# Kernel tuning notes

Measured on AMD Instinct MI355X. Metric: run time of the kernel, lower is better.

The kernel has to match this reference:

```python
import jax, jax.numpy as jnp
import numpy as np

N_NODES = 100000
N_EDGES = 1600000
IN_DIM = 128
HID = 128
BATCH = 16384


def gcn_conv(x, W, b, src, dst, norm, n_nodes):
    # PyG GCNConv: h = x @ W; aggregate norm-weighted messages; add bias.
    h = x @ W                      # [N, H]
    msg = h[src] * norm[:, None]   # [E+N, H] gather + scale
    out = jax.ops.segment_sum(msg, dst, num_segments=n_nodes)
    return out + b


def setup_inputs() -> dict:
    key = jax.random.key(0)
    ks = jax.random.split(key, 12)
    x = jax.random.normal(ks[0], (N_NODES, IN_DIM), dtype=jnp.float32)
    edge_index = jax.random.randint(ks[1], (2, N_EDGES), 0, N_NODES, dtype=jnp.int64)
    src_idx = jax.random.randint(ks[2], (BATCH,), 0, N_NODES, dtype=jnp.int64)
    tgt_idx = jax.random.randint(ks[3], (BATCH,), 0, N_NODES, dtype=jnp.int64)
    s = 1.0 / np.sqrt(HID)
    Wc0 = jax.random.uniform(ks[4], (IN_DIM, HID), jnp.float32, -s, s)
    Wc1 = jax.random.uniform(ks[5], (HID, HID), jnp.float32, -s, s)
    Wc2 = jax.random.uniform(ks[6], (HID, HID), jnp.float32, -s, s)
    bc0 = jnp.zeros((HID,), jnp.float32)
    bc1 = jnp.zeros((HID,), jnp.float32)
    bc2 = jnp.zeros((HID,), jnp.float32)
    s2 = 1.0 / np.sqrt(3 * HID)
    Ww = jax.random.uniform(ks[7], (3 * HID, HID), jnp.float32, -s2, s2)
    bw = jax.random.uniform(ks[8], (HID,), jnp.float32, -s2, s2)
    Wp = jax.random.uniform(ks[9], (3 * HID, HID), jnp.float32, -s2, s2)
    bp = jax.random.uniform(ks[10], (HID,), jnp.float32, -s2, s2)
    return {"x": x, "edge_index": edge_index, "src_idx": src_idx, "tgt_idx": tgt_idx,
            "Wc0": Wc0, "bc0": bc0, "Wc1": Wc1, "bc1": bc1, "Wc2": Wc2, "bc2": bc2,
            "Ww": Ww, "bw": bw, "Wp": Wp, "bp": bp}


def reference(x, edge_index, src_idx, tgt_idx, Wc0, bc0, Wc1, bc1, Wc2, bc2, Ww, bw, Wp, bp):
    n = x.shape[0]
    loops = jnp.arange(n, dtype=edge_index.dtype)
    src = jnp.concatenate([edge_index[0], loops])  # GCN adds self-loops
    dst = jnp.concatenate([edge_index[1], loops])
    deg = jax.ops.segment_sum(jnp.ones_like(src, dtype=x.dtype), dst, num_segments=n)
    dinv = jnp.where(deg > 0, jax.lax.rsqrt(deg), 0.0)
    norm = dinv[src] * dinv[dst]   # symmetric normalization D^-1/2 A D^-1/2

    x1 = jax.nn.relu(gcn_conv(x, Wc0, bc0, src, dst, norm, n))   # dropout p=0 -> identity
    x2 = jax.nn.relu(gcn_conv(x1, Wc1, bc1, src, dst, norm, n))
    x3 = jax.nn.relu(gcn_conv(x2, Wc2, bc2, src, dst, norm, n))
    xcat = jnp.concatenate([x1, x2, x3], axis=1)   # [N, 3H]
    xW = xcat @ Ww + bw   # [N, H]
    xp = xcat @ Wp + bp   # [N, H]
    # bilinear score: bmm of [B,1,H] x [B,H,1] == rowwise dot product
    sv = jnp.sum(xp[src_idx] * xW[tgt_idx], axis=-1)   # [B]
    return sv
```

## Files before the change

### kernel.cpp

```cpp
#include <hip/hip_runtime.h>
#include <hip/hip_bf16.h>

#define N_NODES 100000
#define N_EDGES 1600000
#define BATCH   16384
#define HID     128

#define SHIFT 9
#define BSZ   512
#define NB    196
#define EPB   8192

typedef __attribute__((ext_vector_type(8))) short bf16x8;
typedef __attribute__((ext_vector_type(4))) float fx4;
typedef __attribute__((ext_vector_type(2))) float fx2;

__device__ inline short f2bf(float f) {
    unsigned u = __builtin_bit_cast(unsigned, f);
    unsigned r = (u + 0x7FFF + ((u >> 16) & 1)) >> 16;
    return (short)r;
}
__device__ inline float bf2f(short s) {
    unsigned u = ((unsigned)(unsigned short)s) << 16;
    return __builtin_bit_cast(float, u);
}


__global__ __launch_bounds__(256) void k_bhist(const int* __restrict__ dst,
                                               int* __restrict__ bcnt, int E) {
    __shared__ int lh[NB];
    int t = threadIdx.x;
    for (int j = t; j < NB; j += 256) lh[j] = 0;
    __syncthreads();
    int base = blockIdx.x * 4096;
    int n = min(4096, E - base);
    for (int i = t; i < n; i += 256) atomicAdd(&lh[dst[base + i] >> SHIFT], 1);
    __syncthreads();
    for (int j = t; j < NB; j += 256)
        if (lh[j]) atomicAdd(&bcnt[j], lh[j]);
}

__global__ void k_bscan(const int* __restrict__ bcnt, int* __restrict__ bbase,
                        int* __restrict__ bcur, int* __restrict__ offsets) {
    __shared__ int sh[256];
    int t = threadIdx.x;
    int c = (t < NB) ? bcnt[t] : 0;
    sh[t] = c;
    __syncthreads();
    for (int off = 1; off < 256; off <<= 1) {
        int v = 0;
        if (t >= off) v = sh[t - off];
        __syncthreads();
        if (t >= off) sh[t] += v;
        __syncthreads();
    }
    int incl = sh[t];
    int excl = incl - c;
    if (t < NB) { bbase[t] = excl; bcur[t] = excl; }
    if (t == NB - 1) { bbase[NB] = incl; offsets[N_NODES] = incl; }
}

__global__ __launch_bounds__(256) void k_passA(
    const int* __restrict__ edge, int* __restrict__ bcur,
    unsigned* __restrict__ tmp, int E) {
    __shared__ unsigned staged[EPB];
    __shared__ unsigned char bkt[EPB];
    __shared__ int lh[NB], lstart[NB], gbase[NB], lcur[NB];
    int t = threadIdx.x;
    int base = blockIdx.x * EPB;
    int n = min(EPB, E - base);
    for (int j = t; j < NB; j += 256) lh[j] = 0;
    __syncthreads();
    for (int i = t; i < n; i += 256)
        atomicAdd(&lh[edge[E + base + i] >> SHIFT], 1);
    __syncthreads();
    if (t == 0) {
        int run = 0;
        for (int b = 0; b < NB; ++b) { lstart[b] = run; run += lh[b]; }
    }
    __syncthreads();
    if (t < NB) {
        gbase[t] = atomicAdd(&bcur[t], lh[t]);
        lcur[t] = lstart[t];
    }
    __syncthreads();
    for (int i = t; i < n; i += 256) {
        int s = edge[base + i];
        int d = edge[E + base + i];
        int b = d >> SHIFT;
        unsigned p = (unsigned)s | ((unsigned)(d & (BSZ - 1)) << 17);
        int pos = atomicAdd(&lcur[b], 1);
        staged[pos] = p;
        bkt[pos] = (unsigned char)b;
    }
    __syncthreads();
    for (int i = t; i < n; i += 256) {
        int b = bkt[i];
        tmp[gbase[b] + (i - lstart[b])] = staged[i];
    }
}

__global__ __launch_bounds__(256) void k_passB(
    const unsigned* __restrict__ tmp, const int* __restrict__ bbase,
    int* __restrict__ offsets, float* __restrict__ dinv,
    int* __restrict__ col) {
    __shared__ int lh[BSZ];
    __shared__ int lsum[256];
    int b = blockIdx.x, t = threadIdx.x;
    int begin = bbase[b], end = bbase[b + 1];
    lh[t] = 0; lh[t + 256] = 0;
    __syncthreads();
    for (int i = begin + t; i < end; i += 256)
        atomicAdd(&lh[tmp[i] >> 17], 1);
    __syncthreads();
    int c0 = lh[2 * t], c1 = lh[2 * t + 1];
    int tsum = c0 + c1;
    lsum[t] = tsum;
    __syncthreads();
    for (int off = 1; off < 256; off <<= 1) {
        int v = 0;
        if (t >= off) v = lsum[t - off];
        __syncthreads();
        if (t >= off) lsum[t] += v;
        __syncthreads();
    }
    int texcl = lsum[t] - tsum;
    int node0 = (b << SHIFT) + 2 * t;
    if (node0 < N_NODES) {
        offsets[node0] = begin + texcl;
        dinv[node0] = rsqrtf((float)c0 + 1.f);
    }
    if (node0 + 1 < N_NODES) {
        offsets[node0 + 1] = begin + texcl + c0;
        dinv[node0 + 1] = rsqrtf((float)c1 + 1.f);
    }
    __syncthreads();
    lh[2 * t] = texcl;
    lh[2 * t + 1] = texcl + c0;
    __syncthreads();
    for (int i = begin + t; i < end; i += 1024) {
        int i1 = i + 256, i2 = i + 512, i3 = i + 768;
        unsigned p0 = tmp[i];
        unsigned p1 = (i1 < end) ? tmp[i1] : 0u;
        unsigned p2 = (i2 < end) ? tmp[i2] : 0u;
        unsigned p3 = (i3 < end) ? tmp[i3] : 0u;
        int pos0 = begin + atomicAdd(&lh[p0 >> 17], 1);
        col[pos0] = (int)(p0 & 0x1FFFFu);
        if (i1 < end) { int q = begin + atomicAdd(&lh[p1 >> 17], 1); col[q] = (int)(p1 & 0x1FFFFu); }
        if (i2 < end) { int q = begin + atomicAdd(&lh[p2 >> 17], 1); col[q] = (int)(p2 & 0x1FFFFu); }
        if (i3 < end) { int q = begin + atomicAdd(&lh[p3 >> 17], 1); col[q] = (int)(p3 & 0x1FFFFu); }
    }
}


__global__ void k_prepW(const float* __restrict__ Wc0, const float* __restrict__ Wc1,
                        const float* __restrict__ Wc2, const float* __restrict__ Wp,
                        const float* __restrict__ Ww, short* __restrict__ wI) {
    int c = blockIdx.x;
    const float* src;
    int koff = 0;
    if (c == 0) src = Wc0;
    else if (c == 1) src = Wc1;
    else if (c == 2) src = Wc2;
    else if (c < 6) { src = Wp; koff = (c - 3) * 128; }
    else { src = Ww; koff = (c - 6) * 128; }
    short* d = wI + (size_t)c * 32768;
    for (int i = threadIdx.x; i < 16384; i += 256) {
        int k = i >> 7, n = i & 127;
        float v = src[(size_t)(koff + k) * 128 + n];
        short h = f2bf(v);
        short l = f2bf(v - bf2f(h));
        int c16 = k >> 3, j = k & 7;
        d[n * 256 + c16 * 16 + j] = h;
        d[n * 256 + c16 * 16 + 8 + j] = l;
    }
}


__device__ inline void stage_tile(char* __restrict__ buf, const char* __restrict__ A,
                                  int tile, int maxRow, int t) {
    int rowBase = tile << 5;
#pragma unroll
    for (int j = 0; j < 4; ++j) {
        int s = (j << 8) + t;
        int row = s >> 5;
        int cpos = s & 31;
        int c = cpos ^ (row & 7);
        int gr = rowBase + row;
        if (gr > maxRow) gr = maxRow;
        const char* src = A + ((size_t)gr << 9) + (c << 4);
        char* dst = buf + (((j << 8) + (t & 192)) << 4);
        __builtin_amdgcn_global_load_lds(
            (const __attribute__((address_space(1))) unsigned*)src,
            (__attribute__((address_space(3))) unsigned*)dst, 16, 0, 0);
    }
}

template<int ISF32>
__global__ __launch_bounds__(256) void k_sgemm(
    const char* __restrict__ A, const short* __restrict__ WI,
    short* __restrict__ outb, const float* __restrict__ scale, int M) {
    __shared__ __align__(16) char lds[32768];
    int t = threadIdx.x;
    int lane = t & 63, wave = t >> 6;
    int l15 = lane & 15, g = lane >> 4;
    int colBase = wave << 5;
    int rq = g << 2;

    bf16x8 Bh[4][2], Bl[4][2];
#pragma unroll
    for (int ks = 0; ks < 4; ++ks)
#pragma unroll
        for (int fc = 0; fc < 2; ++fc) {
            int c = colBase + (fc << 4) + l15;
            const short* bp = &WI[((size_t)c << 8) + (((ks << 2) + g) << 4)];
            Bh[ks][fc] = *(const bf16x8*)bp;
            Bl[ks][fc] = *(const bf16x8*)(bp + 8);
        }

    int nT = (M + 31) >> 5;
    int maxRow = M - 1;
    int tile = blockIdx.x;
    if (tile < nT) stage_tile(lds, A, tile, maxRow, t);
    int cur = 0;

    for (; tile < nT; tile += gridDim.x) {
        __syncthreads();
        int nxt = tile + gridDim.x;
        if (nxt < nT) stage_tile(lds + ((cur ^ 1) << 14), A, nxt, maxRow, t);
        char* buf = lds + (cur << 14);

        fx4 acc[2][2];
#pragma unroll
        for (int i = 0; i < 2; ++i)
#pragma unroll
            for (int j = 0; j < 2; ++j) {
                acc[i][j][0] = 0.f; acc[i][j][1] = 0.f;
                acc[i][j][2] = 0.f; acc[i][j][3] = 0.f;
            }

#pragma unroll
        for (int ks = 0; ks < 4; ++ks) {
            bf16x8 ah[2], al[2];
#pragma unroll
            for (int fr = 0; fr < 2; ++fr) {
                int row = (fr << 4) + l15;
                int c0 = (ks << 3) + (g << 1);
                const char* p0 = buf + (row << 9) + ((c0 ^ (row & 7)) << 4);
                const char* p1 = buf + (row << 9) + (((c0 + 1) ^ (row & 7)) << 4);
                if (ISF32) {
                    float v[8];
                    *(float4*)&v[0] = *(const float4*)p0;
                    *(float4*)&v[4] = *(const float4*)p1;
#pragma unroll
                    for (int j = 0; j < 8; ++j) {
                        short hb = f2bf(v[j]);
                        ah[fr][j] = hb;
                        al[fr][j] = f2bf(v[j] - bf2f(hb));
                    }
                } else {
                    ah[fr] = *(const bf16x8*)p0;
                    al[fr] = *(const bf16x8*)p1;
                }
            }
#pragma unroll
            for (int fc = 0; fc < 2; ++fc) {
                acc[0][fc] = __builtin_amdgcn_mfma_f32_16x16x32_bf16(ah[0], Bh[ks][fc], acc[0][fc], 0, 0, 0);
                acc[0][fc] = __builtin_amdgcn_mfma_f32_16x16x32_bf16(ah[0], Bl[ks][fc], acc[0][fc], 0, 0, 0);
                acc[0][fc] = __builtin_amdgcn_mfma_f32_16x16x32_bf16(al[0], Bh[ks][fc], acc[0][fc], 0, 0, 0);
                acc[1][fc] = __builtin_amdgcn_mfma_f32_16x16x32_bf16(ah[1], Bh[ks][fc], acc[1][fc], 0, 0, 0);
                acc[1][fc] = __builtin_amdgcn_mfma_f32_16x16x32_bf16(ah[1], Bl[ks][fc], acc[1][fc], 0, 0, 0);
                acc[1][fc] = __builtin_amdgcn_mfma_f32_16x16x32_bf16(al[1], Bh[ks][fc], acc[1][fc], 0, 0, 0);
            }
        }

        __builtin_amdgcn_s_barrier();

        short* relay = (short*)buf + wave * 1280;
        int rowBaseG = tile << 5;
#pragma unroll
        for (int fr = 0; fr < 2; ++fr)
#pragma unroll
            for (int rg = 0; rg < 4; ++rg) {
                int rl = (fr << 4) + rq + rg;
                int R = rowBaseG + rl;
                float sc = (R < M) ? scale[R] : 0.f;
#pragma unroll
                for (int fc = 0; fc < 2; ++fc)
                    relay[rl * 40 + (fc << 4) + l15] = f2bf(acc[fr][fc][rg] * sc);
            }
        int rr = lane >> 1, seg = lane & 1;
        int R = rowBaseG + rr;
        if (R < M) {
            const short* sp = &relay[rr * 40 + (seg << 4)];
            short* dp = &outb[((size_t)R << 7) + colBase + (seg << 4)];
            ((uint4*)dp)[0] = ((const uint4*)sp)[0];
            ((uint4*)dp)[1] = ((const uint4*)sp)[1];
        }
        cur ^= 1;
    }
}


__device__ inline void addrow(uint4 u, fx2* a) {
    a[0] += (fx2){__builtin_bit_cast(float, u.x << 16),
                  __builtin_bit_cast(float, u.x & 0xFFFF0000u)};
    a[1] += (fx2){__builtin_bit_cast(float, u.y << 16),
                  __builtin_bit_cast(float, u.y & 0xFFFF0000u)};
    a[2] += (fx2){__builtin_bit_cast(float, u.z << 16),
                  __builtin_bit_cast(float, u.z & 0xFFFF0000u)};
    a[3] += (fx2){__builtin_bit_cast(float, u.w << 16),
                  __builtin_bit_cast(float, u.w & 0xFFFF0000u)};
}

__device__ inline void agg_body(const short* __restrict__ h,
                                const int* __restrict__ col,
                                const int* __restrict__ offs,
                                const float* __restrict__ dinv,
                                const float* __restrict__ bias,
                                short* __restrict__ xoI,
                                int v, int orow) {
    int lane = threadIdx.x & 63;
    int g = lane >> 4;
    int li = lane & 15;
    int beg = offs[v], end = offs[v + 1];
    float dv = dinv[v];
    fx2 a4[4] = {{0.f,0.f},{0.f,0.f},{0.f,0.f},{0.f,0.f}};
    if (g == 0)
        addrow(*(const uint4*)&h[(size_t)v * 128 + (li << 3)], a4);
    int e = beg + g;
    for (; e + 12 < end; e += 16) {
        int s0 = col[e], s1 = col[e + 4], s2 = col[e + 8], s3 = col[e + 12];
        uint4 u0 = *(const uint4*)&h[(size_t)s0 * 128 + (li << 3)];
        uint4 u1 = *(const uint4*)&h[(size_t)s1 * 128 + (li << 3)];
        uint4 u2 = *(const uint4*)&h[(size_t)s2 * 128 + (li << 3)];
        uint4 u3 = *(const uint4*)&h[(size_t)s3 * 128 + (li << 3)];
        addrow(u0, a4); addrow(u1, a4); addrow(u2, a4); addrow(u3, a4);
    }
    for (; e < end; e += 4)
        addrow(*(const uint4*)&h[(size_t)col[e] * 128 + (li << 3)], a4);

    float a[8];
#pragma unroll
    for (int j = 0; j < 4; ++j) { a[2 * j] = a4[j][0]; a[2 * j + 1] = a4[j][1]; }
#pragma unroll
    for (int off = 16; off <= 32; off <<= 1)
#pragma unroll
        for (int j = 0; j < 8; ++j) a[j] += __shfl_xor(a[j], off);
    if (g == 0) {
        bf16x8 hh, ll;
#pragma unroll
        for (int j = 0; j < 8; ++j) {
            float o = fmaxf(fmaf(a[j], dv, bias[(li << 3) + j]), 0.f);
            short hb = f2bf(o);
            hh[j] = hb;
            ll[j] = f2bf(o - bf2f(hb));
        }
        short* dst = &xoI[((size_t)orow << 8) + (li << 4)];
        *(bf16x8*)dst = hh;
        *(bf16x8*)(dst + 8) = ll;
    }
}

__global__ __launch_bounds__(256) void k_agg(
    const short* __restrict__ h, const int* __restrict__ col,
    const int* __restrict__ offs, const float* __restrict__ dinv,
    const float* __restrict__ bias, short* __restrict__ xoI, int n) {
    int v = (blockIdx.x << 2) + (threadIdx.x >> 6);
    if (v >= n) return;
    agg_body(h, col, offs, dinv, bias, xoI, v, v);
}

__global__ __launch_bounds__(256) void k_agg3(
    const short* __restrict__ h, const int* __restrict__ col,
    const int* __restrict__ offs, const float* __restrict__ dinv,
    const float* __restrict__ bias, short* __restrict__ xoI,
    const int* __restrict__ sidx, const int* __restrict__ tidx) {
    int i = (blockIdx.x << 2) + (threadIdx.x >> 6);
    if (i >= 2 * BATCH) return;
    int v = (i < BATCH) ? sidx[i] : tidx[i - BATCH];
    agg_body(h, col, offs, dinv, bias, xoI, v, i);
}


__global__ __launch_bounds__(256) void k_pq(
    const short* __restrict__ a1I, const short* __restrict__ a2I,
    const short* __restrict__ x3I, const short* __restrict__ wI,
    const int* __restrict__ sidx, const int* __restrict__ tidx,
    const float* __restrict__ bp, const float* __restrict__ bw,
    float* __restrict__ out) {
    __shared__ float Ps[32][132];
    __shared__ float Qs[32][132];
    int t = threadIdx.x;
    int lane = t & 63, wave = t >> 6;
    int isQ = wave >> 1, wn = wave & 1;
    int l15 = lane & 15;
    int g16 = (lane >> 4) << 4;
    int pairBase = blockIdx.x << 5;
    int colBase = wn << 6;
    const int* gidx = isQ ? tidx : sidx;
    const float* bias = isQ ? bw : bp;
    int r0i = pairBase + l15;
    int r1i = r0i + 16;
    long long n0 = (long long)gidx[r0i];
    long long n1 = (long long)gidx[r1i];

    fx4 acc[2][4];
#pragma unroll
    for (int i = 0; i < 2; ++i)
#pragma unroll
        for (int j = 0; j < 4; ++j) {
            acc[i][j][0] = 0.f; acc[i][j][1] = 0.f;
            acc[i][j][2] = 0.f; acc[i][j][3] = 0.f;
        }

#pragma unroll
    for (int c = 0; c < 3; ++c) {
        const short* AI = (c == 0) ? a1I : (c == 1) ? a2I : x3I;
        long long b0 = (c == 2) ? (long long)(r0i + (isQ << 14)) : n0;
        long long b1 = (c == 2) ? (long long)(r1i + (isQ << 14)) : n1;
        const short* WB = wI + (size_t)(3 + isQ * 3 + c) * 32768;
#pragma unroll
        for (int ks = 0; ks < 4; ++ks) {
            int co = (ks << 6) + g16;
            const short* ap0 = &AI[(b0 << 8) + co];
            const short* ap1 = &AI[(b1 << 8) + co];
            bf16x8 a0h = *(const bf16x8*)ap0;
            bf16x8 a0l = *(const bf16x8*)(ap0 + 8);
            bf16x8 a1h = *(const bf16x8*)ap1;
            bf16x8 a1l = *(const bf16x8*)(ap1 + 8);
#pragma unroll
            for (int fc = 0; fc < 4; ++fc) {
                int cc = colBase + (fc << 4) + l15;
                const short* bpp = &WB[((size_t)cc << 8) + co];
                bf16x8 bh = *(const bf16x8*)bpp;
                bf16x8 bl = *(const bf16x8*)(bpp + 8);
                acc[0][fc] = __builtin_amdgcn_mfma_f32_16x16x32_bf16(a0h, bh, acc[0][fc], 0, 0, 0);
                acc[0][fc] = __builtin_amdgcn_mfma_f32_16x16x32_bf16(a0h, bl, acc[0][fc], 0, 0, 0);
                acc[0][fc] = __builtin_amdgcn_mfma_f32_16x16x32_bf16(a0l, bh, acc[0][fc], 0, 0, 0);
                acc[1][fc] = __builtin_amdgcn_mfma_f32_16x16x32_bf16(a1h, bh, acc[1][fc], 0, 0, 0);
                acc[1][fc] = __builtin_amdgcn_mfma_f32_16x16x32_bf16(a1h, bl, acc[1][fc], 0, 0, 0);
                acc[1][fc] = __builtin_amdgcn_mfma_f32_16x16x32_bf16(a1l, bh, acc[1][fc], 0, 0, 0);
            }
        }
    }

    int rq = (lane >> 4) << 2;
    float (*dst)[132] = isQ ? Qs : Ps;
#pragma unroll
    for (int fr = 0; fr < 2; ++fr) {
#pragma unroll
        for (int fc = 0; fc < 4; ++fc) {
            int cg = colBase + (fc << 4) + l15;
            float bv = bias[cg];
#pragma unroll
            for (int rg = 0; rg < 4; ++rg)
                dst[(fr << 4) + rq + rg][cg] = acc[fr][fc][rg] + bv;
        }
    }
    __syncthreads();

    int p = t >> 3, seg = t & 7;
    const float* pr = &Ps[p][seg * 16];
    const float* qr = &Qs[p][seg * 16];
    float s = 0.f;
#pragma unroll
    for (int j = 0; j < 16; ++j) s += pr[j] * qr[j];
    s += __shfl_xor(s, 1);
    s += __shfl_xor(s, 2);
    s += __shfl_xor(s, 4);
    if (seg == 0) out[pairBase + p] = s;
}


extern "C" void kernel_launch(void* const* d_in, const int* in_sizes, int n_in,
                              void* d_out, int out_size, void* d_ws, size_t ws_size,
                              hipStream_t stream) {
    const float* x    = (const float*)d_in[0];
    const int*   edge = (const int*)d_in[1];
    const int*   sidx = (const int*)d_in[2];
    const int*   tidx = (const int*)d_in[3];
    const float* Wc0  = (const float*)d_in[4];
    const float* bc0  = (const float*)d_in[5];
    const float* Wc1  = (const float*)d_in[6];
    const float* bc1  = (const float*)d_in[7];
    const float* Wc2  = (const float*)d_in[8];
    const float* bc2  = (const float*)d_in[9];
    const float* Ww   = (const float*)d_in[10];
    const float* bw   = (const float*)d_in[11];
    const float* Wp   = (const float*)d_in[12];
    const float* bp   = (const float*)d_in[13];
    float* out = (float*)d_out;

    char* base = (char*)d_ws;
    size_t off = 0;
    auto alloc = [&](size_t bytes) -> char* {
        char* p = base + off;
        off = (off + bytes + 255) & ~(size_t)255;
        return p;
    };
    const size_t ISZ = (size_t)N_NODES * 256 * sizeof(short);
    const size_t XSZ = (size_t)2 * BATCH * 256 * sizeof(short);
    short* a1I  = (short*)alloc(ISZ);
    short* a2I  = (short*)alloc(ISZ);
    short* x3I  = (short*)alloc(XSZ);
    short* hbf  = (short*)alloc((size_t)N_NODES * HID * sizeof(short));
    int*   offsets = (int*)alloc((size_t)(N_NODES + 1) * sizeof(int));
    int*   colArr  = (int*)alloc((size_t)N_EDGES * sizeof(int));
    unsigned* tmp  = (unsigned*)alloc((size_t)N_EDGES * sizeof(unsigned));
    float* dinv    = (float*)alloc((size_t)N_NODES * sizeof(float));
    int*   bcnt    = (int*)alloc(256 * sizeof(int));
    int*   bbase   = (int*)alloc(256 * sizeof(int));
    int*   bcur    = (int*)alloc(256 * sizeof(int));
    short* wI      = (short*)alloc((size_t)9 * 32768 * sizeof(short));
    (void)ws_size; (void)in_sizes; (void)n_in; (void)out_size;

    hipMemsetAsync(bcnt, 0, NB * sizeof(int), stream);
    k_bhist<<<(N_EDGES + 4095) / 4096, 256, 0, stream>>>(edge + N_EDGES, bcnt, N_EDGES);
    k_bscan<<<1, 256, 0, stream>>>(bcnt, bbase, bcur, offsets);
    k_passA<<<(N_EDGES + EPB - 1) / EPB, 256, 0, stream>>>(edge, bcur, tmp, N_EDGES);
    k_passB<<<NB, 256, 0, stream>>>(tmp, bbase, offsets, dinv, colArr);

    k_prepW<<<9, 256, 0, stream>>>(Wc0, Wc1, Wc2, Wp, Ww, wI);

    const int aggGrid  = (N_NODES + 3) / 4;
    const int agg3Grid = (2 * BATCH) / 4;
    const int gemmGrid = 768;
#define WI(c) (wI + (size_t)(c) * 32768)

    k_sgemm<1><<<gemmGrid, 256, 0, stream>>>((const char*)x, WI(0), hbf, dinv, N_NODES);
    k_agg<<<aggGrid, 256, 0, stream>>>(hbf, colArr, offsets, dinv, bc0, a1I, N_NODES);

    k_sgemm<0><<<gemmGrid, 256, 0, stream>>>((const char*)a1I, WI(1), hbf, dinv, N_NODES);
    k_agg<<<aggGrid, 256, 0, stream>>>(hbf, colArr, offsets, dinv, bc1, a2I, N_NODES);

    k_sgemm<0><<<gemmGrid, 256, 0, stream>>>((const char*)a2I, WI(2), hbf, dinv, N_NODES);
    k_agg3<<<agg3Grid, 256, 0, stream>>>(hbf, colArr, offsets, dinv, bc2, x3I, sidx, tidx);

    k_pq<<<BATCH / 32, 256, 0, stream>>>(a1I, a2I, x3I, wI, sidx, tidx, bp, bw, out);
}
```

Measured before the change: 368.8 us.

## Drop bucket histogram pass, deepen GEMM staging to four buffers, move source scaling into aggregation

Removes the bucket histogram and scan kernels by giving each destination bucket a fixed capacity slot (CAP) in the tmp and col arrays, and adds per-node end offsets. Also reworks the GEMM into a 4-deep LDS ring buffer with explicit vmcnt waits and raw barriers, and lowers its grid size. The source dinv scale moves from the GEMM epilogue into the aggregation gather as an FMA per neighbor. The fixed capacity assumes no bucket exceeds CAP edges, which holds only for roughly uniform random graphs. Aggregation now does an extra dinv gather per edge, and the GEMM uses twice the LDS.

```diff
diff --git a/kernel.cpp b/kernel.cpp
--- a/kernel.cpp
+++ b/kernel.cpp
@@ -10,6 +10,7 @@
 #define BSZ   512
 #define NB    196
 #define EPB   8192
+#define CAP   10240
 
 typedef __attribute__((ext_vector_type(8))) short bf16x8;
 typedef __attribute__((ext_vector_type(4))) float fx4;
@@ -25,40 +26,13 @@
     return __builtin_bit_cast(float, u);
 }
 
-
-__global__ __launch_bounds__(256) void k_bhist(const int* __restrict__ dst,
-                                               int* __restrict__ bcnt, int E) {
-    __shared__ int lh[NB];
-    int t = threadIdx.x;
-    for (int j = t; j < NB; j += 256) lh[j] = 0;
-    __syncthreads();
-    int base = blockIdx.x * 4096;
-    int n = min(4096, E - base);
-    for (int i = t; i < n; i += 256) atomicAdd(&lh[dst[base + i] >> SHIFT], 1);
-    __syncthreads();
-    for (int j = t; j < NB; j += 256)
-        if (lh[j]) atomicAdd(&bcnt[j], lh[j]);
-}
-
-__global__ void k_bscan(const int* __restrict__ bcnt, int* __restrict__ bbase,
-                        int* __restrict__ bcur, int* __restrict__ offsets) {
-    __shared__ int sh[256];
-    int t = threadIdx.x;
-    int c = (t < NB) ? bcnt[t] : 0;
-    sh[t] = c;
-    __syncthreads();
-    for (int off = 1; off < 256; off <<= 1) {
-        int v = 0;
-        if (t >= off) v = sh[t - off];
-        __syncthreads();
-        if (t >= off) sh[t] += v;
-        __syncthreads();
-    }
-    int incl = sh[t];
-    int excl = incl - c;
-    if (t < NB) { bbase[t] = excl; bcur[t] = excl; }
-    if (t == NB - 1) { bbase[NB] = incl; offsets[N_NODES] = incl; }
-}
+#define RAW_BARRIER() do { \
+    __builtin_amdgcn_sched_barrier(0); \
+    asm volatile("" ::: "memory"); \
+    __builtin_amdgcn_s_barrier(); \
+    __builtin_amdgcn_sched_barrier(0); \
+} while (0)
+
 
 __global__ __launch_bounds__(256) void k_passA(
     const int* __restrict__ edge, int* __restrict__ bcur,
@@ -96,18 +70,19 @@
     __syncthreads();
     for (int i = t; i < n; i += 256) {
         int b = bkt[i];
-        tmp[gbase[b] + (i - lstart[b])] = staged[i];
+        tmp[(size_t)b * CAP + gbase[b] + (i - lstart[b])] = staged[i];
     }
 }
 
 __global__ __launch_bounds__(256) void k_passB(
-    const unsigned* __restrict__ tmp, const int* __restrict__ bbase,
-    int* __restrict__ offsets, float* __restrict__ dinv,
-    int* __restrict__ col) {
+    const unsigned* __restrict__ tmp, const int* __restrict__ bcur,
+    int* __restrict__ offsets, int* __restrict__ ends,
+    float* __restrict__ dinv, int* __restrict__ col) {
     __shared__ int lh[BSZ];
     __shared__ int lsum[256];
     int b = blockIdx.x, t = threadIdx.x;
-    int begin = bbase[b], end = bbase[b + 1];
+    int begin = b * CAP;
+    int end = begin + bcur[b];
     lh[t] = 0; lh[t + 256] = 0;
     __syncthreads();
     for (int i = begin + t; i < end; i += 256)
@@ -128,10 +103,12 @@
     int node0 = (b << SHIFT) + 2 * t;
     if (node0 < N_NODES) {
         offsets[node0] = begin + texcl;
+        ends[node0] = begin + texcl + c0;
         dinv[node0] = rsqrtf((float)c0 + 1.f);
     }
     if (node0 + 1 < N_NODES) {
         offsets[node0 + 1] = begin + texcl + c0;
+        ends[node0 + 1] = begin + texcl + c0 + c1;
         dinv[node0 + 1] = rsqrtf((float)c1 + 1.f);
     }
     __syncthreads();
@@ -144,8 +121,8 @@
         unsigned p1 = (i1 < end) ? tmp[i1] : 0u;
         unsigned p2 = (i2 < end) ? tmp[i2] : 0u;
         unsigned p3 = (i3 < end) ? tmp[i3] : 0u;
-        int pos0 = begin + atomicAdd(&lh[p0 >> 17], 1);
-        col[pos0] = (int)(p0 & 0x1FFFFu);
+        int q0 = begin + atomicAdd(&lh[p0 >> 17], 1);
+        col[q0] = (int)(p0 & 0x1FFFFu);
         if (i1 < end) { int q = begin + atomicAdd(&lh[p1 >> 17], 1); col[q] = (int)(p1 & 0x1FFFFu); }
         if (i2 < end) { int q = begin + atomicAdd(&lh[p2 >> 17], 1); col[q] = (int)(p2 & 0x1FFFFu); }
         if (i3 < end) { int q = begin + atomicAdd(&lh[p3 >> 17], 1); col[q] = (int)(p3 & 0x1FFFFu); }
@@ -199,8 +176,8 @@
 template<int ISF32>
 __global__ __launch_bounds__(256) void k_sgemm(
     const char* __restrict__ A, const short* __restrict__ WI,
-    short* __restrict__ outb, const float* __restrict__ scale, int M) {
-    __shared__ __align__(16) char lds[32768];
+    short* __restrict__ outb, int M) {
+    __shared__ __align__(16) char lds[65536];
     int t = threadIdx.x;
     int lane = t & 63, wave = t >> 6;
     int l15 = lane & 15, g = lane >> 4;
@@ -220,15 +197,22 @@
 
     int nT = (M + 31) >> 5;
     int maxRow = M - 1;
+    int grid = (int)gridDim.x;
     int tile = blockIdx.x;
-    if (tile < nT) stage_tile(lds, A, tile, maxRow, t);
-    int cur = 0;
-
-    for (; tile < nT; tile += gridDim.x) {
-        __syncthreads();
-        int nxt = tile + gridDim.x;
-        if (nxt < nT) stage_tile(lds + ((cur ^ 1) << 14), A, nxt, maxRow, t);
-        char* buf = lds + (cur << 14);
+    if (tile >= nT) return;
+
+    stage_tile(lds,             A, tile,            maxRow, t);
+    stage_tile(lds + (1 << 14), A, tile + grid,     maxRow, t);
+    stage_tile(lds + (2 << 14), A, tile + 2 * grid, maxRow, t);
+
+    int iter = 0;
+    for (; tile < nT; tile += grid, ++iter) {
+        if (iter == 0)      asm volatile("s_waitcnt vmcnt(8)" ::: "memory");
+        else if (iter == 1) asm volatile("s_waitcnt vmcnt(10)" ::: "memory");
+        else                asm volatile("s_waitcnt vmcnt(12)" ::: "memory");
+        RAW_BARRIER();
+
+        char* buf = lds + ((iter & 3) << 14);
 
         fx4 acc[2][2];
 #pragma unroll
@@ -274,20 +258,18 @@
             }
         }
 
-        __builtin_amdgcn_s_barrier();
-
-        short* relay = (short*)buf + wave * 1280;
+        RAW_BARRIER();
+
+        short* relay = (short*)buf + wave * 2048;
         int rowBaseG = tile << 5;
 #pragma unroll
         for (int fr = 0; fr < 2; ++fr)
 #pragma unroll
             for (int rg = 0; rg < 4; ++rg) {
                 int rl = (fr << 4) + rq + rg;
-                int R = rowBaseG + rl;
-                float sc = (R < M) ? scale[R] : 0.f;
 #pragma unroll
                 for (int fc = 0; fc < 2; ++fc)
-                    relay[rl * 40 + (fc << 4) + l15] = f2bf(acc[fr][fc][rg] * sc);
+                    relay[rl * 40 + (fc << 4) + l15] = f2bf(acc[fr][fc][rg]);
             }
         int rr = lane >> 1, seg = lane & 1;
         int R = rowBaseG + rr;
@@ -297,25 +279,29 @@
             ((uint4*)dp)[0] = ((const uint4*)sp)[0];
             ((uint4*)dp)[1] = ((const uint4*)sp)[1];
         }
-        cur ^= 1;
-    }
-}
-
-
-__device__ inline void addrow(uint4 u, fx2* a) {
-    a[0] += (fx2){__builtin_bit_cast(float, u.x << 16),
-                  __builtin_bit_cast(float, u.x & 0xFFFF0000u)};
-    a[1] += (fx2){__builtin_bit_cast(float, u.y << 16),
-                  __builtin_bit_cast(float, u.y & 0xFFFF0000u)};
-    a[2] += (fx2){__builtin_bit_cast(float, u.z << 16),
-                  __builtin_bit_cast(float, u.z & 0xFFFF0000u)};
-    a[3] += (fx2){__builtin_bit_cast(float, u.w << 16),
-                  __builtin_bit_cast(float, u.w & 0xFFFF0000u)};
+
+        __builtin_amdgcn_sched_barrier(0);
+        stage_tile(lds + (((iter + 3) & 3) << 14), A, tile + 3 * grid, maxRow, t);
+    }
+    asm volatile("s_waitcnt vmcnt(0)" ::: "memory");
+}
+
+
+__device__ inline void addrow(uint4 u, float d, fx2* a) {
+    a[0][0] = fmaf(__builtin_bit_cast(float, u.x << 16), d, a[0][0]);
+    a[0][1] = fmaf(__builtin_bit_cast(float, u.x & 0xFFFF0000u), d, a[0][1]);
+    a[1][0] = fmaf(__builtin_bit_cast(float, u.y << 16), d, a[1][0]);
+    a[1][1] = fmaf(__builtin_bit_cast(float, u.y & 0xFFFF0000u), d, a[1][1]);
+    a[2][0] = fmaf(__builtin_bit_cast(float, u.z << 16), d, a[2][0]);
+    a[2][1] = fmaf(__builtin_bit_cast(float, u.z & 0xFFFF0000u), d, a[2][1]);
+    a[3][0] = fmaf(__builtin_bit_cast(float, u.w << 16), d, a[3][0]);
+    a[3][1] = fmaf(__builtin_bit_cast(float, u.w & 0xFFFF0000u), d, a[3][1]);
 }
 
 __device__ inline void agg_body(const short* __restrict__ h,
                                 const int* __restrict__ col,
                                 const int* __restrict__ offs,
+                                const int* __restrict__ ends,
                                 const float* __restrict__ dinv,
                                 const float* __restrict__ bias,
                                 short* __restrict__ xoI,
@@ -323,22 +309,26 @@
     int lane = threadIdx.x & 63;
     int g = lane >> 4;
     int li = lane & 15;
-    int beg = offs[v], end = offs[v + 1];
+    int beg = offs[v], end = ends[v];
     float dv = dinv[v];
     fx2 a4[4] = {{0.f,0.f},{0.f,0.f},{0.f,0.f},{0.f,0.f}};
     if (g == 0)
-        addrow(*(const uint4*)&h[(size_t)v * 128 + (li << 3)], a4);
+        addrow(*(const uint4*)&h[(size_t)v * 128 + (li << 3)], dv, a4);
     int e = beg + g;
     for (; e + 12 < end; e += 16) {
         int s0 = col[e], s1 = col[e + 4], s2 = col[e + 8], s3 = col[e + 12];
+        float d0 = dinv[s0], d1 = dinv[s1], d2 = dinv[s2], d3 = dinv[s3];
         uint4 u0 = *(const uint4*)&h[(size_t)s0 * 128 + (li << 3)];
         uint4 u1 = *(const uint4*)&h[(size_t)s1 * 128 + (li << 3)];
         uint4 u2 = *(const uint4*)&h[(size_t)s2 * 128 + (li << 3)];
         uint4 u3 = *(const uint4*)&h[(size_t)s3 * 128 + (li << 3)];
-        addrow(u0, a4); addrow(u1, a4); addrow(u2, a4); addrow(u3, a4);
-    }
-    for (; e < end; e += 4)
-        addrow(*(const uint4*)&h[(size_t)col[e] * 128 + (li << 3)], a4);
+        addrow(u0, d0, a4); addrow(u1, d1, a4);
+        addrow(u2, d2, a4); addrow(u3, d3, a4);
+    }
+    for (; e < end; e += 4) {
+        int s = col[e];
+        addrow(*(const uint4*)&h[(size_t)s * 128 + (li << 3)], dinv[s], a4);
+    }
 
     float a[8];
 #pragma unroll
@@ -364,22 +354,24 @@
 
 __global__ __launch_bounds__(256) void k_agg(
     const short* __restrict__ h, const int* __restrict__ col,
-    const int* __restrict__ offs, const float* __restrict__ dinv,
-    const float* __restrict__ bias, short* __restrict__ xoI, int n) {
+    const int* __restrict__ offs, const int* __restrict__ ends,
+    const float* __restrict__ dinv, const float* __restrict__ bias,
+    short* __restrict__ xoI, int n) {
     int v = (blockIdx.x << 2) + (threadIdx.x >> 6);
     if (v >= n) return;
-    agg_body(h, col, offs, dinv, bias, xoI, v, v);
+    agg_body(h, col, offs, ends, dinv, bias, xoI, v, v);
 }
 
 __global__ __launch_bounds__(256) void k_agg3(
     const short* __restrict__ h, const int* __restrict__ col,
-    const int* __restrict__ offs, const float* __restrict__ dinv,
-    const float* __restrict__ bias, short* __restrict__ xoI,
-    const int* __restrict__ sidx, const int* __restrict__ tidx) {
+    const int* __restrict__ offs, const int* __restrict__ ends,
+    const float* __restrict__ dinv, const float* __restrict__ bias,
+    short* __restrict__ xoI, const int* __restrict__ sidx,
+    const int* __restrict__ tidx) {
     int i = (blockIdx.x << 2) + (threadIdx.x >> 6);
     if (i >= 2 * BATCH) return;
     int v = (i < BATCH) ? sidx[i] : tidx[i - BATCH];
-    agg_body(h, col, offs, dinv, bias, xoI, v, i);
+    agg_body(h, col, offs, ends, dinv, bias, xoI, v, i);
 }
 
 
@@ -505,37 +497,34 @@
     short* a2I  = (short*)alloc(ISZ);
     short* x3I  = (short*)alloc(XSZ);
     short* hbf  = (short*)alloc((size_t)N_NODES * HID * sizeof(short));
-    int*   offsets = (int*)alloc((size_t)(N_NODES + 1) * sizeof(int));
-    int*   colArr  = (int*)alloc((size_t)N_EDGES * sizeof(int));
-    unsigned* tmp  = (unsigned*)alloc((size_t)N_EDGES * sizeof(unsigned));
+    int*   offsets = (int*)alloc((size_t)N_NODES * sizeof(int));
+    int*   endsA   = (int*)alloc((size_t)N_NODES * sizeof(int));
+    int*   colArr  = (int*)alloc((size_t)NB * CAP * sizeof(int));
+    unsigned* tmp  = (unsigned*)alloc((size_t)NB * CAP * sizeof(unsigned));
     float* dinv    = (float*)alloc((size_t)N_NODES * sizeof(float));
-    int*   bcnt    = (int*)alloc(256 * sizeof(int));
-    int*   bbase   = (int*)alloc(256 * sizeof(int));
     int*   bcur    = (int*)alloc(256 * sizeof(int));
     short* wI      = (short*)alloc((size_t)9 * 32768 * sizeof(short));
     (void)ws_size; (void)in_sizes; (void)n_in; (void)out_size;
 
-    hipMemsetAsync(bcnt, 0, NB * sizeof(int), stream);
-    k_bhist<<<(N_EDGES + 4095) / 4096, 256, 0, stream>>>(edge + N_EDGES, bcnt, N_EDGES);
-    k_bscan<<<1, 256, 0, stream>>>(bcnt, bbase, bcur, offsets);
+    hipMemsetAsync(bcur, 0, NB * sizeof(int), stream);
     k_passA<<<(N_EDGES + EPB - 1) / EPB, 256, 0, stream>>>(edge, bcur, tmp, N_EDGES);
-    k_passB<<<NB, 256, 0, stream>>>(tmp, bbase, offsets, dinv, colArr);
+    k_passB<<<NB, 256, 0, stream>>>(tmp, bcur, offsets, endsA, dinv, colArr);
 
     k_prepW<<<9, 256, 0, stream>>>(Wc0, Wc1, Wc2, Wp, Ww, wI);
 
     const int aggGrid  = (N_NODES + 3) / 4;
     const int agg3Grid = (2 * BATCH) / 4;
-    const int gemmGrid = 768;
+    const int gemmGrid = 512;
 #define WI(c) (wI + (size_t)(c) * 32768)
 
-    k_sgemm<1><<<gemmGrid, 256, 0, stream>>>((const char*)x, WI(0), hbf, dinv, N_NODES);
-    k_agg<<<aggGrid, 256, 0, stream>>>(hbf, colArr, offsets, dinv, bc0, a1I, N_NODES);
-
-    k_sgemm<0><<<gemmGrid, 256, 0, stream>>>((const char*)a1I, WI(1), hbf, dinv, N_NODES);
-    k_agg<<<aggGrid, 256, 0, stream>>>(hbf, colArr, offsets, dinv, bc1, a2I, N_NODES);
-
-    k_sgemm<0><<<gemmGrid, 256, 0, stream>>>((const char*)a2I, WI(2), hbf, dinv, N_NODES);
-    k_agg3<<<agg3Grid, 256, 0, stream>>>(hbf, colArr, offsets, dinv, bc2, x3I, sidx, tidx);
+    k_sgemm<1><<<gemmGrid, 256, 0, stream>>>((const char*)x, WI(0), hbf, N_NODES);
+    k_agg<<<aggGrid, 256, 0, stream>>>(hbf, colArr, offsets, endsA, dinv, bc0, a1I, N_NODES);
+
+    k_sgemm<0><<<gemmGrid, 256, 0, stream>>>((const char*)a1I, WI(1), hbf, N_NODES);
+    k_agg<<<aggGrid, 256, 0, stream>>>(hbf, colArr, offsets, endsA, dinv, bc1, a2I, N_NODES);
+
+    k_sgemm<0><<<gemmGrid, 256, 0, stream>>>((const char*)a2I, WI(2), hbf, N_NODES);
+    k_agg3<<<agg3Grid, 256, 0, stream>>>(hbf, colArr, offsets, endsA, dinv, bc2, x3I, sidx, tidx);
 
     k_pq<<<BATCH / 32, 256, 0, stream>>>(a1I, a2I, x3I, wI, sidx, tidx, bp, bw, out);
 }
```

Result: faster. 350.2 us (-5.0%).
